# Optimization experiments

Measured on AMD Instinct MI355X. Metric: run time of the kernel, lower is better.

The kernel has to match this reference:

```python
import jax, jax.numpy as jnp
import numpy as np
import math

NUM_HEADS = 16
DIM = 2048
B, N = 4, 1024


def setup_inputs() -> dict:
    key = jax.random.key(0)
    ks = jax.random.split(key, 6)
    s = 1.0 / math.sqrt(DIM)
    return {
        "x": jax.random.normal(ks[0], (B, N, DIM), dtype=jnp.float32),
        "Wqkv": jax.random.normal(ks[1], (3 * DIM, DIM), dtype=jnp.float32) * s,
        "bqkv": jnp.zeros((3 * DIM,), dtype=jnp.float32),
        "Wproj": jax.random.normal(ks[2], (DIM, DIM), dtype=jnp.float32) * s,
        "bproj": jnp.zeros((DIM,), dtype=jnp.float32),
        "noise": jax.random.uniform(ks[3], (B, NUM_HEADS, N, N), dtype=jnp.float32),
    }


def reference(x, Wqkv, bqkv, Wproj, bproj, noise):
    Bb, Nn, C = x.shape
    H = NUM_HEADS
    D = C // H
    # QKV projection: [B, N, 3C] -> [3, B, H, N, D]
    qkv = (x @ Wqkv.T + bqkv).reshape(Bb, Nn, 3, H, D).transpose(2, 0, 3, 1, 4)
    q, k, v = qkv[0], qkv[1], qkv[2]
    # q @ k^T.conj(): q, k are real so conj is identity
    attn = jnp.einsum('bhnd,bhmd->bhnm', q, k) * (1.0 / math.sqrt(D))
    attn = jax.nn.softmax(attn, axis=-1)
    # inject imaginary noise -> complex attention matrix
    attn_c = attn + 1j * noise  # complex64 [B, H, N, N]
    out = jnp.einsum('bhnm,bhmd->bhnd', attn_c, v.astype(attn_c.dtype))
    out = out.transpose(0, 2, 1, 3).reshape(Bb, Nn, C)  # [B, N, C] complex
    # real-weight linear on complex input, then take real part
    out = out @ Wproj.T.astype(out.dtype) + bproj
    return out.real
```

## Files before the change

### kernel.cpp

```cpp
#include <hip/hip_runtime.h>
#include <hip/hip_bf16.h>
#include <math.h>

typedef __attribute__((ext_vector_type(8))) short bf16x8;
typedef __attribute__((ext_vector_type(4))) float f32x4;

static constexpr int kB = 4, kN = 1024, kC = 2048, kH = 16, kD = 128;
static constexpr int kM = kB * kN;
static constexpr int k3C = 3 * kC;

__device__ __forceinline__ short f2bf(float f) {
  unsigned u = __float_as_uint(f);
  u = (u + 0x7FFFu + ((u >> 16) & 1u)) >> 16;
  return (short)u;
}

__global__ __launch_bounds__(256) void cast_f32_bf16(const float* __restrict__ in,
                                                     short* __restrict__ out, int n4) {
  int stride = gridDim.x * blockDim.x;
  for (int i = blockIdx.x * blockDim.x + threadIdx.x; i < n4; i += stride) {
    float4 v = reinterpret_cast<const float4*>(in)[i];
    short4 o = make_short4(f2bf(v.x), f2bf(v.y), f2bf(v.z), f2bf(v.w));
    reinterpret_cast<short4*>(out)[i] = o;
  }
}

template <int EPI>
__global__ __launch_bounds__(256) void gemm_bt(const short* __restrict__ A,
                                               const short* __restrict__ Bt,
                                               const float* __restrict__ bias,
                                               void* __restrict__ out0,
                                               short* __restrict__ vT,
                                               int M, int N, int K) {
  __shared__ __align__(16) short As[2][128 * 32];
  __shared__ __align__(16) short Bs[2][128 * 32];
  const int lane = threadIdx.x & 63;
  const int wid = threadIdx.x >> 6;
  const int row0 = blockIdx.x * 128;
  const int col0 = blockIdx.y * 128;
  const int wrow = (wid >> 1) * 64;
  const int wcol = (wid & 1) * 64;
  f32x4 acc[4][4] = {};

  const int skc = (lane & 3) ^ ((lane >> 3) & 3);
  const short* Ag0 = A + (size_t)(row0 + wid * 32 + (lane >> 2)) * K + skc * 8;
  const short* Bg0 = Bt + (size_t)(col0 + wid * 32 + (lane >> 2)) * K + skc * 8;

#define GSTAGE(buf, k0)                                                                 \
  {                                                                                     \
    __builtin_amdgcn_global_load_lds(                                                   \
        (const __attribute__((address_space(1))) void*)(Ag0 + (k0)),                    \
        (__attribute__((address_space(3))) void*)&As[buf][(wid * 32) * 32], 16, 0, 0);  \
    __builtin_amdgcn_global_load_lds(                                                   \
        (const __attribute__((address_space(1))) void*)(Ag0 + 16 * (size_t)K + (k0)),   \
        (__attribute__((address_space(3))) void*)&As[buf][(wid * 32 + 16) * 32], 16, 0, \
        0);                                                                             \
    __builtin_amdgcn_global_load_lds(                                                   \
        (const __attribute__((address_space(1))) void*)(Bg0 + (k0)),                    \
        (__attribute__((address_space(3))) void*)&Bs[buf][(wid * 32) * 32], 16, 0, 0);  \
    __builtin_amdgcn_global_load_lds(                                                   \
        (const __attribute__((address_space(1))) void*)(Bg0 + 16 * (size_t)K + (k0)),   \
        (__attribute__((address_space(3))) void*)&Bs[buf][(wid * 32 + 16) * 32], 16, 0, \
        0);                                                                             \
  }

  GSTAGE(0, 0);
  __syncthreads();

  int cur = 0;
  for (int k0 = 0; k0 < K; k0 += 32) {
    if (k0 + 32 < K) GSTAGE(cur ^ 1, k0 + 32);

    const char* abase = (const char*)&As[cur][0];
    const char* bbase = (const char*)&Bs[cur][0];
    bf16x8 af[4], bfr[4];
#pragma unroll
    for (int mt = 0; mt < 4; ++mt) {
      const int row = wrow + mt * 16 + (lane & 15);
      af[mt] = *(const bf16x8*)(abase + row * 64 +
                                (((lane >> 4) ^ ((row >> 1) & 3)) << 4));
    }
#pragma unroll
    for (int nt = 0; nt < 4; ++nt) {
      const int col = wcol + nt * 16 + (lane & 15);
      bfr[nt] = *(const bf16x8*)(bbase + col * 64 +
                                 (((lane >> 4) ^ ((col >> 1) & 3)) << 4));
    }
#pragma unroll
    for (int mt = 0; mt < 4; ++mt)
#pragma unroll
      for (int nt = 0; nt < 4; ++nt)
        acc[mt][nt] = __builtin_amdgcn_mfma_f32_16x16x32_bf16(af[mt], bfr[nt], acc[mt][nt], 0, 0, 0);

    __syncthreads();
    cur ^= 1;
  }
#undef GSTAGE

  if (EPI == 0) {
    short* qk = (short*)out0;
#pragma unroll
    for (int mt = 0; mt < 4; ++mt) {
#pragma unroll
      for (int nt = 0; nt < 4; ++nt) {
        int col = col0 + wcol + nt * 16 + (lane & 15);
        float bv = bias[col];
#pragma unroll
        for (int r = 0; r < 4; ++r) {
          int row = row0 + wrow + mt * 16 + (lane >> 4) * 4 + r;
          float v = acc[mt][nt][r] + bv;
          if (col < 4096) {
            qk[(size_t)row * 4096 + col] = f2bf(v);
          } else {
            int b = row >> 10, pos = row & 1023;
            int hd = col - 4096;
            vT[((size_t)b * 2048 + hd) * 1024 + pos] = f2bf(v);
          }
        }
      }
    }
  } else {
    float* out = (float*)out0;
#pragma unroll
    for (int mt = 0; mt < 4; ++mt) {
#pragma unroll
      for (int nt = 0; nt < 4; ++nt) {
        int col = col0 + wcol + nt * 16 + (lane & 15);
        float bv = bias[col];
#pragma unroll
        for (int r = 0; r < 4; ++r) {
          int row = row0 + wrow + mt * 16 + (lane >> 4) * 4 + r;
          out[(size_t)row * N + col] = acc[mt][nt][r] + bv;
        }
      }
    }
  }
}

__global__ __launch_bounds__(256) void attn_kernel(const short* __restrict__ qk,
                                                   const short* __restrict__ vT,
                                                   short* __restrict__ att) {
  __shared__ __align__(16) short Ks[2][64][128];
  __shared__ __align__(16) short Vs[2][128][64];
  __shared__ __align__(16) short P[4][16][72];
  const int lane = threadIdx.x & 63;
  const int wid = threadIdx.x >> 6;
  const int bh = blockIdx.y;
  const int b = bh >> 4, h = bh & 15;
  const int q0 = blockIdx.x * 64 + wid * 16;

  const short* qbase = qk + (size_t)(b * 1024) * 4096 + h * 128;
  const short* kglob = qbase + 2048;
  const short* vglob = vT + (size_t)bh * 128 * 1024;

  bf16x8 qf[4];
  {
    const int qrow = q0 + (lane & 15);
#pragma unroll
    for (int dc = 0; dc < 4; ++dc)
      qf[dc] = *(const bf16x8*)&qbase[(size_t)qrow * 4096 + dc * 32 + (lane >> 4) * 8];
  }

  const int krow_l = wid * 16 + (lane >> 4);
  const int kcol_l = (lane & 15) << 4;
  const int vrow_l = wid * 32 + (lane >> 3);
  const int vcol_l = (lane & 7) << 4;

#define STAGE_KV(buf, kv0)                                                              \
  {                                                                                     \
    _Pragma("unroll") for (int i = 0; i < 4; ++i) {                                     \
      int r = krow_l + i * 4;                                                           \
      const char* src = (const char*)(kglob + (size_t)((kv0) + r) * 4096) +             \
                        (kcol_l ^ ((r & 7) << 4));                                      \
      __builtin_amdgcn_global_load_lds(                                                 \
          (const __attribute__((address_space(1))) void*)src,                           \
          (__attribute__((address_space(3))) void*)&Ks[buf][wid * 16 + i * 4][0], 16,   \
          0, 0);                                                                        \
    }                                                                                   \
    _Pragma("unroll") for (int i = 0; i < 4; ++i) {                                     \
      int d = vrow_l + i * 8;                                                           \
      const char* src = (const char*)(vglob + (size_t)d * 1024 + (kv0)) +               \
                        (vcol_l ^ ((d & 7) << 4));                                      \
      __builtin_amdgcn_global_load_lds(                                                 \
          (const __attribute__((address_space(1))) void*)src,                           \
          (__attribute__((address_space(3))) void*)&Vs[buf][wid * 32 + i * 8][0], 16,   \
          0, 0);                                                                        \
    }                                                                                   \
  }

  float l_r[4] = {0.f, 0.f, 0.f, 0.f};
  f32x4 accO[8] = {};

  const float scale = 0.08838834764831845f;

  STAGE_KV(0, 0);
  asm volatile("s_waitcnt vmcnt(0)" ::: "memory");
  __builtin_amdgcn_s_barrier();
  __builtin_amdgcn_sched_barrier(0);

  int cur = 0;
  for (int t = 0; t < 16; ++t) {
    if (t < 15) STAGE_KV(cur ^ 1, (t + 1) * 64);

    f32x4 s4[4] = {};
#pragma unroll
    for (int kt = 0; kt < 4; ++kt) {
      const int row = kt * 16 + (lane & 15);
      const char* kr = (const char*)&Ks[cur][row][0];
      const int swz = (row & 7) << 4;
#pragma unroll
      for (int dc = 0; dc < 4; ++dc) {
        bf16x8 kf = *(const bf16x8*)(kr + ((dc * 64 + (lane >> 4) * 16) ^ swz));
        s4[kt] = __builtin_amdgcn_mfma_f32_16x16x32_bf16(qf[dc], kf, s4[kt], 0, 0, 0);
      }
    }

#pragma unroll
    for (int r = 0; r < 4; ++r) {
      float p0 = __expf(s4[0][r] * scale);
      float p1 = __expf(s4[1][r] * scale);
      float p2 = __expf(s4[2][r] * scale);
      float p3 = __expf(s4[3][r] * scale);
      l_r[r] += (p0 + p1) + (p2 + p3);
      int prow = (lane >> 4) * 4 + r;
      P[wid][prow][(lane & 15)] = f2bf(p0);
      P[wid][prow][16 + (lane & 15)] = f2bf(p1);
      P[wid][prow][32 + (lane & 15)] = f2bf(p2);
      P[wid][prow][48 + (lane & 15)] = f2bf(p3);
    }

    bf16x8 pf0 = *(const bf16x8*)&P[wid][lane & 15][(lane >> 4) * 8];
    bf16x8 pf1 = *(const bf16x8*)&P[wid][lane & 15][32 + (lane >> 4) * 8];

#pragma unroll
    for (int d0 = 0; d0 < 8; ++d0) {
      const int d = d0 * 16 + (lane & 15);
      const char* vr = (const char*)&Vs[cur][d][0];
      const int swz = (d & 7) << 4;
      bf16x8 vf0 = *(const bf16x8*)(vr + (((lane >> 4) * 16) ^ swz));
      bf16x8 vf1 = *(const bf16x8*)(vr + ((64 + (lane >> 4) * 16) ^ swz));
      accO[d0] = __builtin_amdgcn_mfma_f32_16x16x32_bf16(pf0, vf0, accO[d0], 0, 0, 0);
      accO[d0] = __builtin_amdgcn_mfma_f32_16x16x32_bf16(pf1, vf1, accO[d0], 0, 0, 0);
    }

    asm volatile("s_waitcnt vmcnt(0)" ::: "memory");
    __builtin_amdgcn_s_barrier();
    __builtin_amdgcn_sched_barrier(0);
    cur ^= 1;
  }
#undef STAGE_KV

  float invl[4];
#pragma unroll
  for (int r = 0; r < 4; ++r) {
    float s = l_r[r];
#pragma unroll
    for (int off = 1; off < 16; off <<= 1) s += __shfl_xor(s, off);
    invl[r] = 1.0f / s;
  }
#pragma unroll
  for (int d0 = 0; d0 < 8; ++d0) {
#pragma unroll
    for (int r = 0; r < 4; ++r) {
      int arow = q0 + (lane >> 4) * 4 + r;
      att[(size_t)(b * 1024 + arow) * 2048 + h * 128 + d0 * 16 + (lane & 15)] =
          f2bf(accO[d0][r] * invl[r]);
    }
  }
}

extern "C" void kernel_launch(void* const* d_in, const int* in_sizes, int n_in,
                              void* d_out, int out_size, void* d_ws, size_t ws_size,
                              hipStream_t stream) {
  const float* x = (const float*)d_in[0];
  const float* Wqkv = (const float*)d_in[1];
  const float* bqkv = (const float*)d_in[2];
  const float* Wproj = (const float*)d_in[3];
  const float* bproj = (const float*)d_in[4];
  float* out = (float*)d_out;

  char* ws = (char*)d_ws;
  short* xb = (short*)(ws + 0);
  short* Wqkvb = (short*)(ws + 16777216);
  short* Wprojb = (short*)(ws + 41943040);
  short* qkbuf = (short*)(ws + 50331648);
  short* vT = (short*)(ws + 83886080);
  short* attb = (short*)(ws + 100663296);

  hipLaunchKernelGGL(cast_f32_bf16, dim3(2048), dim3(256), 0, stream,
                     x, xb, kM * kC / 4);
  hipLaunchKernelGGL(cast_f32_bf16, dim3(2048), dim3(256), 0, stream,
                     Wqkv, Wqkvb, k3C * kC / 4);
  hipLaunchKernelGGL(cast_f32_bf16, dim3(2048), dim3(256), 0, stream,
                     Wproj, Wprojb, kC * kC / 4);

  hipLaunchKernelGGL((gemm_bt<0>), dim3(kM / 128, k3C / 128), dim3(256), 0, stream,
                     xb, Wqkvb, bqkv, (void*)qkbuf, vT, kM, k3C, kC);

  hipLaunchKernelGGL(attn_kernel, dim3(kN / 64, kB * kH), dim3(256), 0, stream,
                     qkbuf, vT, attb);

  hipLaunchKernelGGL((gemm_bt<1>), dim3(kM / 128, kC / 128), dim3(256), 0, stream,
                     attb, Wprojb, bproj, (void*)out, (short*)nullptr, kM, kC, kC);
}
```

Baseline: 280.5 us.

## Rework GEMM into 8-wave, 4-stage LDS pipeline with explicit vmcnt waits

Both projection GEMMs now run 512-thread blocks of 8 waves, each wave computing a 64x32 subtile instead of 64x64. The LDS pipeline is deepened from double buffering to four stages with three tiles in flight, using explicit s_waitcnt vmcnt counts and raw s_barrier in place of __syncthreads. MFMA sections are wrapped in s_setprio to favour matrix issue. The aim is to hide global-load latency and raise occupancy, at the cost of more LDS per block (64KB), extra barriers per iteration, and less register reuse per wave.

Result: slower. 288.7 us (+2.9%).

```diff
diff --git a/kernel.cpp b/kernel.cpp
--- a/kernel.cpp
+++ b/kernel.cpp
@@ -26,88 +26,100 @@
 }
 
 template <int EPI>
-__global__ __launch_bounds__(256) void gemm_bt(const short* __restrict__ A,
-                                               const short* __restrict__ Bt,
-                                               const float* __restrict__ bias,
-                                               void* __restrict__ out0,
-                                               short* __restrict__ vT,
-                                               int M, int N, int K) {
-  __shared__ __align__(16) short As[2][128 * 32];
-  __shared__ __align__(16) short Bs[2][128 * 32];
+__global__ __launch_bounds__(512, 4) void gemm_p4(const short* __restrict__ A,
+                                                  const short* __restrict__ Bt,
+                                                  const float* __restrict__ bias,
+                                                  void* __restrict__ out0,
+                                                  short* __restrict__ vT,
+                                                  int M, int N, int K) {
+  __shared__ __align__(16) short As[4][128 * 32];
+  __shared__ __align__(16) short Bs[4][128 * 32];
   const int lane = threadIdx.x & 63;
   const int wid = threadIdx.x >> 6;
+  const int wr = wid >> 2;
+  const int wc = wid & 3;
   const int row0 = blockIdx.x * 128;
   const int col0 = blockIdx.y * 128;
-  const int wrow = (wid >> 1) * 64;
-  const int wcol = (wid & 1) * 64;
-  f32x4 acc[4][4] = {};
 
   const int skc = (lane & 3) ^ ((lane >> 3) & 3);
-  const short* Ag0 = A + (size_t)(row0 + wid * 32 + (lane >> 2)) * K + skc * 8;
-  const short* Bg0 = Bt + (size_t)(col0 + wid * 32 + (lane >> 2)) * K + skc * 8;
-
-#define GSTAGE(buf, k0)                                                                 \
+  const short* Ag = A + (size_t)(row0 + wid * 16 + (lane >> 2)) * K + skc * 8;
+  const short* Bg = Bt + (size_t)(col0 + wid * 16 + (lane >> 2)) * K + skc * 8;
+
+  f32x4 acc[4][2] = {};
+
+#define PSTAGE(buf, k0)                                                                 \
   {                                                                                     \
     __builtin_amdgcn_global_load_lds(                                                   \
-        (const __attribute__((address_space(1))) void*)(Ag0 + (k0)),                    \
-        (__attribute__((address_space(3))) void*)&As[buf][(wid * 32) * 32], 16, 0, 0);  \
+        (const __attribute__((address_space(1))) void*)(Ag + (k0)),                     \
+        (__attribute__((address_space(3))) void*)&As[buf][(wid * 16) * 32], 16, 0, 0);  \
     __builtin_amdgcn_global_load_lds(                                                   \
-        (const __attribute__((address_space(1))) void*)(Ag0 + 16 * (size_t)K + (k0)),   \
-        (__attribute__((address_space(3))) void*)&As[buf][(wid * 32 + 16) * 32], 16, 0, \
-        0);                                                                             \
-    __builtin_amdgcn_global_load_lds(                                                   \
-        (const __attribute__((address_space(1))) void*)(Bg0 + (k0)),                    \
-        (__attribute__((address_space(3))) void*)&Bs[buf][(wid * 32) * 32], 16, 0, 0);  \
-    __builtin_amdgcn_global_load_lds(                                                   \
-        (const __attribute__((address_space(1))) void*)(Bg0 + 16 * (size_t)K + (k0)),   \
-        (__attribute__((address_space(3))) void*)&Bs[buf][(wid * 32 + 16) * 32], 16, 0, \
-        0);                                                                             \
-  }
-
-  GSTAGE(0, 0);
-  __syncthreads();
-
-  int cur = 0;
-  for (int k0 = 0; k0 < K; k0 += 32) {
-    if (k0 + 32 < K) GSTAGE(cur ^ 1, k0 + 32);
-
-    const char* abase = (const char*)&As[cur][0];
-    const char* bbase = (const char*)&Bs[cur][0];
-    bf16x8 af[4], bfr[4];
+        (const __attribute__((address_space(1))) void*)(Bg + (k0)),                     \
+        (__attribute__((address_space(3))) void*)&Bs[buf][(wid * 16) * 32], 16, 0, 0);  \
+  }
+
+  const int NT = K >> 5;
+  PSTAGE(0, 0);
+  PSTAGE(1, 32);
+  PSTAGE(2, 64);
+  asm volatile("s_waitcnt vmcnt(4)" ::: "memory");
+  __builtin_amdgcn_s_barrier();
+  __builtin_amdgcn_sched_barrier(0);
+
+  for (int t = 0; t < NT; ++t) {
+    const int buf = t & 3;
+    if (t + 3 < NT) {
+      PSTAGE((t + 3) & 3, (t + 3) * 32);
+      asm volatile("s_waitcnt vmcnt(6)" ::: "memory");
+    } else if (t + 2 < NT) {
+      asm volatile("s_waitcnt vmcnt(4)" ::: "memory");
+    } else if (t + 1 < NT) {
+      asm volatile("s_waitcnt vmcnt(2)" ::: "memory");
+    } else {
+      asm volatile("s_waitcnt vmcnt(0)" ::: "memory");
+    }
+    __builtin_amdgcn_s_barrier();
+    __builtin_amdgcn_sched_barrier(0);
+
+    const char* abase = (const char*)&As[buf][0];
+    const char* bbase = (const char*)&Bs[buf][0];
+    bf16x8 af[4], bfr[2];
 #pragma unroll
     for (int mt = 0; mt < 4; ++mt) {
-      const int row = wrow + mt * 16 + (lane & 15);
+      const int row = wr * 64 + mt * 16 + (lane & 15);
       af[mt] = *(const bf16x8*)(abase + row * 64 +
                                 (((lane >> 4) ^ ((row >> 1) & 3)) << 4));
     }
 #pragma unroll
-    for (int nt = 0; nt < 4; ++nt) {
-      const int col = wcol + nt * 16 + (lane & 15);
+    for (int nt = 0; nt < 2; ++nt) {
+      const int col = wc * 32 + nt * 16 + (lane & 15);
       bfr[nt] = *(const bf16x8*)(bbase + col * 64 +
                                  (((lane >> 4) ^ ((col >> 1) & 3)) << 4));
     }
+    __builtin_amdgcn_s_setprio(1);
 #pragma unroll
     for (int mt = 0; mt < 4; ++mt)
 #pragma unroll
-      for (int nt = 0; nt < 4; ++nt)
+      for (int nt = 0; nt < 2; ++nt)
         acc[mt][nt] = __builtin_amdgcn_mfma_f32_16x16x32_bf16(af[mt], bfr[nt], acc[mt][nt], 0, 0, 0);
-
-    __syncthreads();
-    cur ^= 1;
-  }
-#undef GSTAGE
+    __builtin_amdgcn_s_setprio(0);
+
+    asm volatile("s_waitcnt lgkmcnt(0)" ::: "memory");
+    __builtin_amdgcn_s_barrier();
+    __builtin_amdgcn_sched_barrier(0);
+  }
+#undef PSTAGE
 
   if (EPI == 0) {
     short* qk = (short*)out0;
 #pragma unroll
     for (int mt = 0; mt < 4; ++mt) {
 #pragma unroll
-      for (int nt = 0; nt < 4; ++nt) {
-        int col = col0 + wcol + nt * 16 + (lane & 15);
+      for (int nt = 0; nt < 2; ++nt) {
+        int col = col0 + wc * 32 + nt * 16 + (lane & 15);
         float bv = bias[col];
 #pragma unroll
         for (int r = 0; r < 4; ++r) {
-          int row = row0 + wrow + mt * 16 + (lane >> 4) * 4 + r;
+          int row = row0 + wr * 64 + mt * 16 + (lane >> 4) * 4 + r;
           float v = acc[mt][nt][r] + bv;
           if (col < 4096) {
             qk[(size_t)row * 4096 + col] = f2bf(v);
@@ -124,12 +136,12 @@
 #pragma unroll
     for (int mt = 0; mt < 4; ++mt) {
 #pragma unroll
-      for (int nt = 0; nt < 4; ++nt) {
-        int col = col0 + wcol + nt * 16 + (lane & 15);
+      for (int nt = 0; nt < 2; ++nt) {
+        int col = col0 + wc * 32 + nt * 16 + (lane & 15);
         float bv = bias[col];
 #pragma unroll
         for (int r = 0; r < 4; ++r) {
-          int row = row0 + wrow + mt * 16 + (lane >> 4) * 4 + r;
+          int row = row0 + wr * 64 + mt * 16 + (lane >> 4) * 4 + r;
           out[(size_t)row * N + col] = acc[mt][nt][r] + bv;
         }
       }
@@ -294,12 +306,12 @@
   hipLaunchKernelGGL(cast_f32_bf16, dim3(2048), dim3(256), 0, stream,
                      Wproj, Wprojb, kC * kC / 4);
 
-  hipLaunchKernelGGL((gemm_bt<0>), dim3(kM / 128, k3C / 128), dim3(256), 0, stream,
+  hipLaunchKernelGGL((gemm_p4<0>), dim3(kM / 128, k3C / 128), dim3(512), 0, stream,
                      xb, Wqkvb, bqkv, (void*)qkbuf, vT, kM, k3C, kC);
 
   hipLaunchKernelGGL(attn_kernel, dim3(kN / 64, kB * kH), dim3(256), 0, stream,
                      qkbuf, vT, attb);
 
-  hipLaunchKernelGGL((gemm_bt<1>), dim3(kM / 128, kC / 128), dim3(256), 0, stream,
+  hipLaunchKernelGGL((gemm_p4<1>), dim3(kM / 128, kC / 128), dim3(512), 0, stream,
                      attb, Wprojb, bproj, (void*)out, (short*)nullptr, kM, kC, kC);
 }
```

## Use two-wave 128x128 GEMM blocks with 64x128 per-wave tiles

Applied to the files above, without the earlier changes.

The GEMM kernel drops from four waves (each computing a 64x64 sub-tile) to two waves per 128x128 block, each computing a 64x128 sub-tile with 32 accumulator fragments. The aim is better register-level reuse, since each A fragment feeds eight MFMAs instead of four, and fewer LDS reads per MFMA. In exchange each wave needs many more accumulator registers and each block has fewer waves, which can reduce latency hiding. Launch bounds are set to allow two blocks per CU.

New measurement: 302.5 us. +7.8%, slower.

```diff
diff --git a/kernel.cpp b/kernel.cpp
--- a/kernel.cpp
+++ b/kernel.cpp
@@ -26,42 +26,41 @@
 }
 
 template <int EPI>
-__global__ __launch_bounds__(256) void gemm_bt(const short* __restrict__ A,
-                                               const short* __restrict__ Bt,
-                                               const float* __restrict__ bias,
-                                               void* __restrict__ out0,
-                                               short* __restrict__ vT,
-                                               int M, int N, int K) {
+__global__ __launch_bounds__(128, 2) void gemm_w2(const short* __restrict__ A,
+                                                  const short* __restrict__ Bt,
+                                                  const float* __restrict__ bias,
+                                                  void* __restrict__ out0,
+                                                  short* __restrict__ vT,
+                                                  int M, int N, int K) {
   __shared__ __align__(16) short As[2][128 * 32];
   __shared__ __align__(16) short Bs[2][128 * 32];
   const int lane = threadIdx.x & 63;
   const int wid = threadIdx.x >> 6;
   const int row0 = blockIdx.x * 128;
   const int col0 = blockIdx.y * 128;
-  const int wrow = (wid >> 1) * 64;
-  const int wcol = (wid & 1) * 64;
-  f32x4 acc[4][4] = {};
 
   const int skc = (lane & 3) ^ ((lane >> 3) & 3);
-  const short* Ag0 = A + (size_t)(row0 + wid * 32 + (lane >> 2)) * K + skc * 8;
-  const short* Bg0 = Bt + (size_t)(col0 + wid * 32 + (lane >> 2)) * K + skc * 8;
+  const short* Ag = A + (size_t)(row0 + wid * 64 + (lane >> 2)) * K + skc * 8;
+  const short* Bg = Bt + (size_t)(col0 + wid * 64 + (lane >> 2)) * K + skc * 8;
+
+  f32x4 acc[4][8] = {};
 
 #define GSTAGE(buf, k0)                                                                 \
   {                                                                                     \
-    __builtin_amdgcn_global_load_lds(                                                   \
-        (const __attribute__((address_space(1))) void*)(Ag0 + (k0)),                    \
-        (__attribute__((address_space(3))) void*)&As[buf][(wid * 32) * 32], 16, 0, 0);  \
-    __builtin_amdgcn_global_load_lds(                                                   \
-        (const __attribute__((address_space(1))) void*)(Ag0 + 16 * (size_t)K + (k0)),   \
-        (__attribute__((address_space(3))) void*)&As[buf][(wid * 32 + 16) * 32], 16, 0, \
-        0);                                                                             \
-    __builtin_amdgcn_global_load_lds(                                                   \
-        (const __attribute__((address_space(1))) void*)(Bg0 + (k0)),                    \
-        (__attribute__((address_space(3))) void*)&Bs[buf][(wid * 32) * 32], 16, 0, 0);  \
-    __builtin_amdgcn_global_load_lds(                                                   \
-        (const __attribute__((address_space(1))) void*)(Bg0 + 16 * (size_t)K + (k0)),   \
-        (__attribute__((address_space(3))) void*)&Bs[buf][(wid * 32 + 16) * 32], 16, 0, \
-        0);                                                                             \
+    _Pragma("unroll") for (int i = 0; i < 4; ++i) {                                     \
+      __builtin_amdgcn_global_load_lds(                                                 \
+          (const __attribute__((address_space(1))) void*)(Ag + (size_t)i * 16 * K +     \
+                                                          (k0)),                        \
+          (__attribute__((address_space(3))) void*)&As[buf][(wid * 64 + i * 16) * 32],  \
+          16, 0, 0);                                                                    \
+    }                                                                                   \
+    _Pragma("unroll") for (int i = 0; i < 4; ++i) {                                     \
+      __builtin_amdgcn_global_load_lds(                                                 \
+          (const __attribute__((address_space(1))) void*)(Bg + (size_t)i * 16 * K +     \
+                                                          (k0)),                        \
+          (__attribute__((address_space(3))) void*)&Bs[buf][(wid * 64 + i * 16) * 32],  \
+          16, 0, 0);                                                                    \
+    }                                                                                   \
   }
 
   GSTAGE(0, 0);
@@ -73,24 +72,24 @@
 
     const char* abase = (const char*)&As[cur][0];
     const char* bbase = (const char*)&Bs[cur][0];
-    bf16x8 af[4], bfr[4];
+    bf16x8 af[4], bf[8];
 #pragma unroll
     for (int mt = 0; mt < 4; ++mt) {
-      const int row = wrow + mt * 16 + (lane & 15);
+      const int row = wid * 64 + mt * 16 + (lane & 15);
       af[mt] = *(const bf16x8*)(abase + row * 64 +
                                 (((lane >> 4) ^ ((row >> 1) & 3)) << 4));
     }
 #pragma unroll
-    for (int nt = 0; nt < 4; ++nt) {
-      const int col = wcol + nt * 16 + (lane & 15);
-      bfr[nt] = *(const bf16x8*)(bbase + col * 64 +
-                                 (((lane >> 4) ^ ((col >> 1) & 3)) << 4));
+    for (int nt = 0; nt < 8; ++nt) {
+      const int col = nt * 16 + (lane & 15);
+      bf[nt] = *(const bf16x8*)(bbase + col * 64 +
+                                (((lane >> 4) ^ ((col >> 1) & 3)) << 4));
     }
 #pragma unroll
     for (int mt = 0; mt < 4; ++mt)
 #pragma unroll
-      for (int nt = 0; nt < 4; ++nt)
-        acc[mt][nt] = __builtin_amdgcn_mfma_f32_16x16x32_bf16(af[mt], bfr[nt], acc[mt][nt], 0, 0, 0);
+      for (int nt = 0; nt < 8; ++nt)
+        acc[mt][nt] = __builtin_amdgcn_mfma_f32_16x16x32_bf16(af[mt], bf[nt], acc[mt][nt], 0, 0, 0);
 
     __syncthreads();
     cur ^= 1;
@@ -102,12 +101,12 @@
 #pragma unroll
     for (int mt = 0; mt < 4; ++mt) {
 #pragma unroll
-      for (int nt = 0; nt < 4; ++nt) {
-        int col = col0 + wcol + nt * 16 + (lane & 15);
+      for (int nt = 0; nt < 8; ++nt) {
+        int col = col0 + nt * 16 + (lane & 15);
         float bv = bias[col];
 #pragma unroll
         for (int r = 0; r < 4; ++r) {
-          int row = row0 + wrow + mt * 16 + (lane >> 4) * 4 + r;
+          int row = row0 + wid * 64 + mt * 16 + (lane >> 4) * 4 + r;
           float v = acc[mt][nt][r] + bv;
           if (col < 4096) {
             qk[(size_t)row * 4096 + col] = f2bf(v);
@@ -124,12 +123,12 @@
 #pragma unroll
     for (int mt = 0; mt < 4; ++mt) {
 #pragma unroll
-      for (int nt = 0; nt < 4; ++nt) {
-        int col = col0 + wcol + nt * 16 + (lane & 15);
+      for (int nt = 0; nt < 8; ++nt) {
+        int col = col0 + nt * 16 + (lane & 15);
         float bv = bias[col];
 #pragma unroll
         for (int r = 0; r < 4; ++r) {
-          int row = row0 + wrow + mt * 16 + (lane >> 4) * 4 + r;
+          int row = row0 + wid * 64 + mt * 16 + (lane >> 4) * 4 + r;
           out[(size_t)row * N + col] = acc[mt][nt][r] + bv;
         }
       }
@@ -294,12 +293,12 @@
   hipLaunchKernelGGL(cast_f32_bf16, dim3(2048), dim3(256), 0, stream,
                      Wproj, Wprojb, kC * kC / 4);
 
-  hipLaunchKernelGGL((gemm_bt<0>), dim3(kM / 128, k3C / 128), dim3(256), 0, stream,
+  hipLaunchKernelGGL((gemm_w2<0>), dim3(kM / 128, k3C / 128), dim3(128), 0, stream,
                      xb, Wqkvb, bqkv, (void*)qkbuf, vT, kM, k3C, kC);
 
   hipLaunchKernelGGL(attn_kernel, dim3(kN / 64, kB * kH), dim3(256), 0, stream,
                      qkbuf, vT, attb);
 
-  hipLaunchKernelGGL((gemm_bt<1>), dim3(kM / 128, kC / 128), dim3(256), 0, stream,
+  hipLaunchKernelGGL((gemm_w2<1>), dim3(kM / 128, kC / 128), dim3(128), 0, stream,
                      attb, Wprojb, bproj, (void*)out, (short*)nullptr, kM, kC, kC);
 }
```

## Replace QKV GEMM with 256x256-tile, 4-stage direct-to-LDS pipelined kernel

Applied to the files above, without the earlier changes.

Adds a new QKV projection GEMM that uses 256x256 output tiles with 512 threads and a 4-deep LDS ring filled by global_load_lds. LDS rows are XOR-swizzled, and MFMA phases are wrapped in s_setprio. The goal is more reuse per tile and better hiding of global load latency than the previous 128x128 double-buffered kernel. In exchange it uses much more LDS (128 KB), which limits occupancy, and the epilogue still writes the transposed V with scattered stores.

Measured after the change: 326.2 us. +16.3%, slower.

```diff
diff --git a/kernel.cpp b/kernel.cpp
--- a/kernel.cpp
+++ b/kernel.cpp
@@ -22,6 +22,118 @@
     float4 v = reinterpret_cast<const float4*>(in)[i];
     short4 o = make_short4(f2bf(v.x), f2bf(v.y), f2bf(v.z), f2bf(v.w));
     reinterpret_cast<short4*>(out)[i] = o;
+  }
+}
+
+__global__ __launch_bounds__(512, 2) void gemm_v5(const short* __restrict__ A,
+                                                  const short* __restrict__ Bt,
+                                                  const float* __restrict__ bias,
+                                                  short* __restrict__ qk,
+                                                  short* __restrict__ vT,
+                                                  int M, int N, int K) {
+  __shared__ __align__(16) short As[4][256 * 32];
+  __shared__ __align__(16) short Bs[4][256 * 32];
+  const int lane = threadIdx.x & 63;
+  const int wid = threadIdx.x >> 6;
+  const int wr = wid >> 2;
+  const int wc = wid & 3;
+  const int row0 = blockIdx.x * 256;
+  const int col0 = blockIdx.y * 256;
+
+  const int rs = wid * 16 + (lane >> 2);
+  const int csrc = (lane & 3) ^ ((rs >> 1) & 3);
+  const short* Ag0 = A + (size_t)(row0 + rs) * K + csrc * 8;
+  const short* Ag1 = A + (size_t)(row0 + 128 + rs) * K + csrc * 8;
+  const short* Bg0 = Bt + (size_t)(col0 + rs) * K + csrc * 8;
+  const short* Bg1 = Bt + (size_t)(col0 + 128 + rs) * K + csrc * 8;
+
+  f32x4 acc[8][4] = {};
+
+#define VSTAGE(buf, t)                                                                  \
+  {                                                                                     \
+    const int k0 = (t) * 32;                                                            \
+    __builtin_amdgcn_global_load_lds(                                                   \
+        (const __attribute__((address_space(1))) void*)(Ag0 + k0),                      \
+        (__attribute__((address_space(3))) void*)&As[buf][(wid * 16) * 32], 16, 0, 0);  \
+    __builtin_amdgcn_global_load_lds(                                                   \
+        (const __attribute__((address_space(1))) void*)(Ag1 + k0),                      \
+        (__attribute__((address_space(3))) void*)&As[buf][(128 + wid * 16) * 32], 16,   \
+        0, 0);                                                                          \
+    __builtin_amdgcn_global_load_lds(                                                   \
+        (const __attribute__((address_space(1))) void*)(Bg0 + k0),                      \
+        (__attribute__((address_space(3))) void*)&Bs[buf][(wid * 16) * 32], 16, 0, 0);  \
+    __builtin_amdgcn_global_load_lds(                                                   \
+        (const __attribute__((address_space(1))) void*)(Bg1 + k0),                      \
+        (__attribute__((address_space(3))) void*)&Bs[buf][(128 + wid * 16) * 32], 16,   \
+        0, 0);                                                                          \
+  }
+
+  const int NT = K >> 5;
+  VSTAGE(0, 0);
+  VSTAGE(1, 1);
+  VSTAGE(2, 2);
+  asm volatile("s_waitcnt vmcnt(8)" ::: "memory");
+  __builtin_amdgcn_s_barrier();
+  __builtin_amdgcn_sched_barrier(0);
+
+  for (int t = 0; t < NT; ++t) {
+    const int buf = t & 3;
+    const bool more = (t + 3 < NT);
+    if (more) VSTAGE((t + 3) & 3, t + 3);
+
+    const char* abase = (const char*)&As[buf][0];
+    const char* bbase = (const char*)&Bs[buf][0];
+    bf16x8 af[8], bfv[4];
+#pragma unroll
+    for (int mt = 0; mt < 8; ++mt) {
+      const int row = wr * 128 + mt * 16 + (lane & 15);
+      af[mt] = *(const bf16x8*)(abase + row * 64 +
+                                (((lane >> 4) ^ ((row >> 1) & 3)) << 4));
+    }
+#pragma unroll
+    for (int nt = 0; nt < 4; ++nt) {
+      const int colr = wc * 64 + nt * 16 + (lane & 15);
+      bfv[nt] = *(const bf16x8*)(bbase + colr * 64 +
+                                 (((lane >> 4) ^ ((colr >> 1) & 3)) << 4));
+    }
+    __builtin_amdgcn_s_setprio(1);
+#pragma unroll
+    for (int mt = 0; mt < 8; ++mt)
+#pragma unroll
+      for (int nt = 0; nt < 4; ++nt)
+        acc[mt][nt] = __builtin_amdgcn_mfma_f32_16x16x32_bf16(af[mt], bfv[nt], acc[mt][nt], 0, 0, 0);
+    __builtin_amdgcn_s_setprio(0);
+
+    if (more)
+      asm volatile("s_waitcnt vmcnt(8) lgkmcnt(0)" ::: "memory");
+    else if (t + 2 < NT)
+      asm volatile("s_waitcnt vmcnt(4) lgkmcnt(0)" ::: "memory");
+    else
+      asm volatile("s_waitcnt vmcnt(0) lgkmcnt(0)" ::: "memory");
+    __builtin_amdgcn_s_barrier();
+    __builtin_amdgcn_sched_barrier(0);
+  }
+#undef VSTAGE
+
+#pragma unroll
+  for (int mt = 0; mt < 8; ++mt) {
+#pragma unroll
+    for (int nt = 0; nt < 4; ++nt) {
+      int col = col0 + wc * 64 + nt * 16 + (lane & 15);
+      float bv = bias[col];
+#pragma unroll
+      for (int r = 0; r < 4; ++r) {
+        int row = row0 + wr * 128 + mt * 16 + (lane >> 4) * 4 + r;
+        float v = acc[mt][nt][r] + bv;
+        if (col < 4096) {
+          qk[(size_t)row * 4096 + col] = f2bf(v);
+        } else {
+          int b = row >> 10, pos = row & 1023;
+          int hd = col - 4096;
+          vT[((size_t)b * 2048 + hd) * 1024 + pos] = f2bf(v);
+        }
+      }
+    }
   }
 }
 
@@ -294,8 +406,8 @@
   hipLaunchKernelGGL(cast_f32_bf16, dim3(2048), dim3(256), 0, stream,
                      Wproj, Wprojb, kC * kC / 4);
 
-  hipLaunchKernelGGL((gemm_bt<0>), dim3(kM / 128, k3C / 128), dim3(256), 0, stream,
-                     xb, Wqkvb, bqkv, (void*)qkbuf, vT, kM, k3C, kC);
+  hipLaunchKernelGGL(gemm_v5, dim3(kM / 256, k3C / 256), dim3(512), 0, stream,
+                     xb, Wqkvb, bqkv, qkbuf, vT, kM, k3C, kC);
 
   hipLaunchKernelGGL(attn_kernel, dim3(kN / 64, kB * kH), dim3(256), 0, stream,
                      qkbuf, vT, attb);
```
